# Performance work log

Hardware: AMD Instinct MI355X
Metric: run time of the kernel (lower is better)

## Reference

```python
import jax, jax.numpy as jnp
import numpy as np

D_MODEL = 512
N_HEADS = 8
HEAD_DIM = D_MODEL // N_HEADS
NEG_INF = -1e9


def setup_inputs() -> dict:
    key = jax.random.key(0)
    ks = jax.random.split(key, 12)
    B, N, M = 8, 2048, 2048
    inp = {
        'query': jax.random.normal(ks[0], (B, D_MODEL, N), jnp.float32),
        'key': jax.random.normal(ks[1], (B, D_MODEL, M), jnp.float32),
        'value': jax.random.normal(ks[2], (B, D_MODEL, M), jnp.float32),
        'query_mask': jnp.ones((B, N), jnp.float32),
        'key_value_mask': jnp.ones((B, M), jnp.float32),
        # Conv1d(d_model, d_model, kernel_size=1) == pointwise linear: W [out, in], b [out]
        'Wq': jax.random.normal(ks[3], (D_MODEL, D_MODEL), jnp.float32) / np.sqrt(D_MODEL),
        'bq': jax.random.normal(ks[4], (D_MODEL,), jnp.float32) * 0.01,
        'Wk': jax.random.normal(ks[5], (D_MODEL, D_MODEL), jnp.float32) / np.sqrt(D_MODEL),
        'bk': jax.random.normal(ks[6], (D_MODEL,), jnp.float32) * 0.01,
        'Wv': jax.random.normal(ks[7], (D_MODEL, D_MODEL), jnp.float32) / np.sqrt(D_MODEL),
        'bv': jax.random.normal(ks[8], (D_MODEL,), jnp.float32) * 0.01,
        'Wm': jax.random.normal(ks[9], (D_MODEL, D_MODEL), jnp.float32) / np.sqrt(D_MODEL),
        'bm': jax.random.normal(ks[10], (D_MODEL,), jnp.float32) * 0.01,
    }
    return inp


def _pointwise(W, b, x):
    # Conv1d k=1 over [B, C_in, N] -> [B, C_out, N]
    return jnp.einsum('oi,bin->bon', W, x) + b[None, :, None]


def reference(query, key, value, query_mask, key_value_mask,
              Wq, bq, Wk, bk, Wv, bv, Wm, bm):
    B = query.shape[0]
    N = query.shape[2]
    M = key.shape[2]
    # project and split heads: [B, head_dim, n_heads, seq]
    q = _pointwise(Wq, bq, query).reshape(B, HEAD_DIM, N_HEADS, N)
    k = _pointwise(Wk, bk, key).reshape(B, HEAD_DIM, N_HEADS, M)
    v = _pointwise(Wv, bv, value).reshape(B, HEAD_DIM, N_HEADS, M)
    # scores [B, H, N, M], scaled by sqrt(head_dim) (query.shape[1] post-split)
    scores = jnp.einsum('bdhn,bdhm->bhnm', q, k) / jnp.sqrt(jnp.float32(HEAD_DIM))
    # dual mask: outer product of key_value_mask [B,1,1,M] and query_mask [B,1,N,1]
    mask = key_value_mask[:, None, None, :] * query_mask[:, None, :, None]
    scores = jnp.where(mask > 0, scores, NEG_INF)
    prob = jax.nn.softmax(scores, axis=-1)  # [B, H, N, M]
    x = jnp.einsum('bhnm,bdhm->bdhn', prob, v)  # [B, head_dim, H, N]
    out = _pointwise(Wm, bm, x.reshape(B, D_MODEL, N))
    return out
```

## Files before the change

kernel.cpp:

```cpp
#include <hip/hip_runtime.h>


typedef _Float16 f16;
typedef _Float16 f16x4 __attribute__((ext_vector_type(4)));
typedef _Float16 f16x8 __attribute__((ext_vector_type(8)));
typedef float f32x4 __attribute__((ext_vector_type(4)));

#define D_MODEL 512
#define HD 64
#define SEQ 2048
#define QSCL 0.18033688011112042f
#define KVNEG -1.4426950409e9f
#define FMAXB -6.0f

__global__ __launch_bounds__(256) void k_transpose(
    const float* __restrict__ q, const float* __restrict__ k, const float* __restrict__ v,
    f16* __restrict__ XT)
{
  __shared__ __align__(16) f16 Ts[64][72];
  int t = threadIdx.x;
  int nt = blockIdx.x, ct = blockIdx.y, z = blockIdx.z;
  int src = z >> 3, b = z & 7;
  const float* S = (src == 0) ? q : (src == 1) ? k : v;
  {
    int cr = t >> 2, ns = t & 3;
    const float* p = S + ((size_t)b * D_MODEL + ct * 64 + cr) * SEQ + nt * 64 + ns * 16;
    f32x4 a0 = *(const f32x4*)(p);
    f32x4 a1 = *(const f32x4*)(p + 4);
    f32x4 a2 = *(const f32x4*)(p + 8);
    f32x4 a3 = *(const f32x4*)(p + 12);
    f16x8 h0, h1;
#pragma unroll
    for (int j = 0; j < 4; ++j) { h0[j] = (f16)a0[j]; h0[4 + j] = (f16)a1[j]; h1[j] = (f16)a2[j]; h1[4 + j] = (f16)a3[j]; }
    *(f16x8*)&Ts[cr][ns * 16] = h0;
    *(f16x8*)&Ts[cr][ns * 16 + 8] = h1;
  }
  __syncthreads();
  {
    int nr = t >> 2, cs = t & 3;
    f16x8 h0, h1;
#pragma unroll
    for (int j = 0; j < 8; ++j) h0[j] = Ts[cs * 16 + j][nr];
#pragma unroll
    for (int j = 0; j < 8; ++j) h1[j] = Ts[cs * 16 + 8 + j][nr];
    f16* dst = XT + (((size_t)z) * SEQ + nt * 64 + nr) * D_MODEL + ct * 64 + cs * 16;
    *(f16x8*)dst = h0;
    *(f16x8*)(dst + 8) = h1;
  }
}

__global__ __launch_bounds__(256) void k_wconv(
    const float* __restrict__ Wq, const float* __restrict__ Wk, const float* __restrict__ Wv,
    const float* __restrict__ Wm, f16* __restrict__ W3, f16* __restrict__ Wmh)
{
  int idx = blockIdx.x * 256 + threadIdx.x;
  if (idx < 262144) {
    W3[idx] = (f16)Wq[idx];
    W3[262144 + idx] = (f16)Wk[idx];
    W3[524288 + idx] = (f16)Wv[idx];
    int o = idx >> 9, c = idx & 511;
    int h = c & 7, d = c >> 3;
    Wmh[((size_t)h * 512 + o) * 64 + d] = (f16)Wm[idx];
  }
}

__global__ __launch_bounds__(256, 2) void k_proj(
    const f16* __restrict__ W3, const float* __restrict__ bq, const float* __restrict__ bk,
    const float* __restrict__ bv, const f16* __restrict__ XT,
    f16* __restrict__ Qt, f16* __restrict__ Kt, f16* __restrict__ Vh)
{
  __shared__ __align__(16) char smem[36864];
  f16 (*As)[72] = (f16(*)[72])smem;
  f16 (*Bs)[72] = (f16(*)[72])(smem + 18432);
  f16 (*Ls)[136] = (f16(*)[136])smem;

  int t = threadIdx.x;
  int proj = blockIdx.z, b = blockIdx.y;
  int ot = blockIdx.x & 3, ntile = blockIdx.x >> 2;
  int w = t >> 6, ln = t & 63, i16 = ln & 15, q4 = ln >> 4;
  int ow = w >> 1, nw = w & 1;

  const f16* Wp = W3 + (size_t)proj * 262144;
  const f16* Xp = XT + ((size_t)proj * 8 + b) * (size_t)SEQ * D_MODEL;

  f32x4 acc[4][4];
#pragma unroll
  for (int x = 0; x < 4; ++x)
#pragma unroll
    for (int y = 0; y < 4; ++y) acc[x][y] = (f32x4){0.f, 0.f, 0.f, 0.f};

  int srow = t >> 1, shalf = t & 1;
  for (int kc = 0; kc < 8; ++kc) {
    __syncthreads();
    const f16* Ap = Wp + ((size_t)(ot * 128 + srow)) * 512 + kc * 64 + shalf * 32;
#pragma unroll
    for (int s8 = 0; s8 < 4; ++s8)
      *(f32x4*)&As[srow][shalf * 32 + s8 * 8] = *(const f32x4*)(Ap + s8 * 8);
    const f16* Bp = Xp + ((size_t)(ntile * 128 + srow)) * 512 + kc * 64 + shalf * 32;
#pragma unroll
    for (int s8 = 0; s8 < 4; ++s8)
      *(f32x4*)&Bs[srow][shalf * 32 + s8 * 8] = *(const f32x4*)(Bp + s8 * 8);
    __syncthreads();
#pragma unroll
    for (int kk = 0; kk < 2; ++kk) {
      f16x8 af[4], bf[4];
#pragma unroll
      for (int x = 0; x < 4; ++x) af[x] = *(const f16x8*)&As[ow * 64 + x * 16 + i16][kk * 32 + q4 * 8];
#pragma unroll
      for (int y = 0; y < 4; ++y) bf[y] = *(const f16x8*)&Bs[nw * 64 + y * 16 + i16][kk * 32 + q4 * 8];
#pragma unroll
      for (int x = 0; x < 4; ++x)
#pragma unroll
        for (int y = 0; y < 4; ++y)
          acc[x][y] = __builtin_amdgcn_mfma_f32_16x16x32_f16(af[x], bf[y], acc[x][y], 0, 0, 0);
    }
  }

  const float* bias = (proj == 0) ? bq : (proj == 1) ? bk : bv;
  float scl = (proj == 0) ? QSCL : 1.0f;
  __syncthreads();
#pragma unroll
  for (int x = 0; x < 4; ++x) {
    f32x4 bb = *(const f32x4*)(bias + ot * 128 + ow * 64 + x * 16 + q4 * 4);
#pragma unroll
    for (int y = 0; y < 4; ++y)
#pragma unroll
      for (int r = 0; r < 4; ++r)
        Ls[ow * 64 + x * 16 + q4 * 4 + r][nw * 64 + y * 16 + i16] = (f16)((acc[x][y][r] + bb[r]) * scl);
  }
  __syncthreads();
  if (proj < 2) {
    f16* dst = (proj == 0) ? Qt : Kt;
    int n = t >> 1, seg = t & 1;
#pragma unroll
    for (int h = 0; h < 8; ++h) {
      f16x8 g;
#pragma unroll
      for (int j = 0; j < 8; ++j) g[j] = Ls[8 * (seg * 8 + j) + h][n];
      f16* dp = dst + (((size_t)((b * 8 + h) * 4 + ot)) * 2048 + ntile * 128 + n) * 16 + seg * 8;
      *(f16x8*)dp = g;
    }
  } else {
#pragma unroll
    for (int p = 0; p < 8; ++p) {
      int ol = (t >> 4) + 16 * p;
      int ch = t & 15;
      int og = ot * 128 + ol;
      int h = og & 7, d = og >> 3;
      f16* dp = Vh + (((size_t)(b * 8 + h)) * HD + d) * SEQ + ntile * 128 + ch * 8;
      *(f32x4*)dp = *(const f32x4*)&Ls[ol][ch * 8];
    }
  }
}

__global__ __launch_bounds__(256, 4) void k_attn(
    const f16* __restrict__ Qt, const f16* __restrict__ Kt, const f16* __restrict__ Vh,
    const float* __restrict__ qmask, const float* __restrict__ kvmask,
    f16* __restrict__ O)
{
  __shared__ __align__(16) char smem[18432];
  f16 (*Qs)[72] = (f16(*)[72])smem;
  f16 (*Ks)[72] = (f16(*)[72])smem;
  f16 (*Vs)[72] = (f16(*)[72])(smem + 9216);

  int t = threadIdx.x;
  int bh = blockIdx.x >> 4;
  int b = bh >> 3;
  int n0 = (blockIdx.x & 15) * 128;
  int w = t >> 6, ln = t & 63, i16 = ln & 15, q4 = ln >> 4;

  const f16* Qb = Qt + (size_t)bh * 131072;
  const f16* Kb = Kt + (size_t)bh * 131072;
  const f16* Vb = Vh + (size_t)bh * HD * SEQ;
  const float* kvp = kvmask + (size_t)b * SEQ;

  int tid0 = t, tid1 = 256 + t;
  int cx0 = tid0 >> 6, nk0 = tid0 & 63;
  int cx1 = tid1 >> 6, nk1 = tid1 & 63;
  int rk0 = (nk0 & 32) | ((nk0 & 4) << 2) | ((nk0 >> 1) & 12) | (nk0 & 3);
  int rk1 = (nk1 & 32) | ((nk1 & 4) << 2) | ((nk1 >> 1) & 12) | (nk1 & 3);
  int vw0 = tid0 >> 3, vc0 = tid0 & 7;
  int vw1 = tid1 >> 3, vc1 = tid1 & 7;
  const f16* ksp0 = Kb + ((size_t)((cx0 >> 1) * 2048 + nk0)) * 16 + (cx0 & 1) * 8;
  const f16* ksp1 = Kb + ((size_t)((cx1 >> 1) * 2048 + nk1)) * 16 + (cx1 & 1) * 8;
  const f16* vsp0 = Vb + (size_t)vw0 * SEQ + vc0 * 8;
  const f16* vsp1 = Vb + (size_t)vw1 * SEQ + vc1 * 8;

  f32x4 kA = *(const f32x4*)(ksp0);
  f32x4 kB = *(const f32x4*)(ksp1);
  f32x4 vA = *(const f32x4*)(vsp0);
  f32x4 vB = *(const f32x4*)(vsp1);

#pragma unroll
  for (int p = 0; p < 4; ++p) {
    int tid = p * 256 + t;
    int n = tid & 127, cx = tid >> 7;
    *(f32x4*)&Qs[n][cx * 8] =
        *(const f32x4*)(Qb + ((size_t)((cx >> 1) * 2048 + n0 + n)) * 16 + (cx & 1) * 8);
  }
  __syncthreads();
  f16x8 qf[2][2];
#pragma unroll
  for (int nt = 0; nt < 2; ++nt)
#pragma unroll
    for (int kc = 0; kc < 2; ++kc)
      qf[nt][kc] = *(const f16x8*)&Qs[w * 32 + nt * 16 + i16][kc * 32 + q4 * 8];
#pragma unroll
  for (int nt = 0; nt < 2; ++nt) {
    float qok = qmask[(size_t)b * SEQ + n0 + w * 32 + nt * 16 + i16];
    f16 qz = (qok > 0.f) ? (f16)1 : (f16)0;
    qf[nt][0] *= qz;
    qf[nt][1] *= qz;
  }

  f32x4 acc_o[4][2];
#pragma unroll
  for (int dt = 0; dt < 4; ++dt)
#pragma unroll
    for (int nt = 0; nt < 2; ++nt) acc_o[dt][nt] = (f32x4){0.f, 0.f, 0.f, 0.f};
  float rsum2[2] = {0.f, 0.f};

  for (int it = 0; it < 32; ++it) {
    int m0 = it * 64;
    __syncthreads();
    *(f32x4*)&Ks[rk0][cx0 * 8] = kA;
    *(f32x4*)&Ks[rk1][cx1 * 8] = kB;
    *(f32x4*)&Vs[vw0][vc0 * 8] = vA;
    *(f32x4*)&Vs[vw1][vc1 * 8] = vB;
    __syncthreads();
    if (it < 31) {
      int mo = (it + 1) * 64;
      kA = *(const f32x4*)(ksp0 + (size_t)mo * 16);
      kB = *(const f32x4*)(ksp1 + (size_t)mo * 16);
      vA = *(const f32x4*)(vsp0 + mo);
      vB = *(const f32x4*)(vsp1 + mo);
    }

    f32x4 bias[4];
#pragma unroll
    for (int mt = 0; mt < 4; ++mt) {
      f32x4 kv = *(const f32x4*)(kvp + m0 + ((mt >> 1) << 5) + ((mt & 1) << 2) + q4 * 8);
#pragma unroll
      for (int r = 0; r < 4; ++r) bias[mt][r] = (kv[r] > 0.f) ? FMAXB : KVNEG;
    }

    f32x4 s[2][4];
    __builtin_amdgcn_s_setprio(1);
#pragma unroll
    for (int mt = 0; mt < 4; ++mt) {
      f16x8 kf0 = *(const f16x8*)&Ks[mt * 16 + i16][q4 * 8];
      f16x8 kf1 = *(const f16x8*)&Ks[mt * 16 + i16][32 + q4 * 8];
      f32x4 a0 = __builtin_amdgcn_mfma_f32_16x16x32_f16(kf0, qf[0][0], bias[mt], 0, 0, 0);
      s[0][mt] = __builtin_amdgcn_mfma_f32_16x16x32_f16(kf1, qf[0][1], a0, 0, 0, 0);
      f32x4 a1 = __builtin_amdgcn_mfma_f32_16x16x32_f16(kf0, qf[1][0], bias[mt], 0, 0, 0);
      s[1][mt] = __builtin_amdgcn_mfma_f32_16x16x32_f16(kf1, qf[1][1], a1, 0, 0, 0);
    }
    __builtin_amdgcn_s_setprio(0);

    f16x8 pf[2][2];
#pragma unroll
    for (int nt = 0; nt < 2; ++nt) {
      float rs = 0.f;
#pragma unroll
      for (int mtp = 0; mtp < 2; ++mtp) {
        f16x8 pv;
#pragma unroll
        for (int r = 0; r < 4; ++r) {
          float p0 = __builtin_amdgcn_exp2f(s[nt][2 * mtp][r]);
          float p1 = __builtin_amdgcn_exp2f(s[nt][2 * mtp + 1][r]);
          rs += p0 + p1;
          pv[r] = (f16)p0;
          pv[4 + r] = (f16)p1;
        }
        pf[mtp][nt] = pv;
      }
      rsum2[nt] += rs;
    }

    __builtin_amdgcn_s_setprio(1);
#pragma unroll
    for (int dt = 0; dt < 4; ++dt) {
      f16x8 vf0 = *(const f16x8*)&Vs[dt * 16 + i16][q4 * 8];
      f16x8 vf1 = *(const f16x8*)&Vs[dt * 16 + i16][32 + q4 * 8];
#pragma unroll
      for (int nt = 0; nt < 2; ++nt) {
        f32x4 o = acc_o[dt][nt];
        o = __builtin_amdgcn_mfma_f32_16x16x32_f16(vf0, pf[0][nt], o, 0, 0, 0);
        o = __builtin_amdgcn_mfma_f32_16x16x32_f16(vf1, pf[1][nt], o, 0, 0, 0);
        acc_o[dt][nt] = o;
      }
    }
    __builtin_amdgcn_s_setprio(0);
  }

  __syncthreads();
  f16 (*Os)[72] = (f16(*)[72])(smem + w * 4608);
#pragma unroll
  for (int nt = 0; nt < 2; ++nt) {
    float l = rsum2[nt];
    l += __shfl_xor(l, 16, 64);
    l += __shfl_xor(l, 32, 64);
    float inv = 1.f / l;
#pragma unroll
    for (int dt = 0; dt < 4; ++dt) {
      f16x4 o4;
#pragma unroll
      for (int r = 0; r < 4; ++r) o4[r] = (f16)(acc_o[dt][nt][r] * inv);
      *(f16x4*)&Os[nt * 16 + i16][dt * 16 + q4 * 4] = o4;
    }
  }
  __syncthreads();
  f16* Ob = O + ((size_t)bh * SEQ + n0 + w * 32) * HD;
#pragma unroll
  for (int p = 0; p < 4; ++p) {
    int row = (ln >> 3) + 8 * p, ch = ln & 7;
    *(f32x4*)(Ob + (size_t)row * HD + ch * 8) = *(const f32x4*)&Os[row][ch * 8];
  }
}

__global__ __launch_bounds__(256, 2) void k_out(
    const f16* __restrict__ Wmh, const float* __restrict__ bm,
    const f16* __restrict__ O, float* __restrict__ out)
{
  __shared__ __align__(16) char smem[20480];
  f16 (*As)[40] = (f16(*)[40])smem;
  f16 (*Bs)[40] = (f16(*)[40])(smem + 10240);

  int t = threadIdx.x;
  int b = blockIdx.y;
  int ot = blockIdx.x & 3, ntile = blockIdx.x >> 2;
  int w = t >> 6, ln = t & 63, i16 = ln & 15, q4 = ln >> 4;
  int ow = w >> 1, nw = w & 1;

  f32x4 acc[4][4];
#pragma unroll
  for (int x = 0; x < 4; ++x)
#pragma unroll
    for (int y = 0; y < 4; ++y) acc[x][y] = (f32x4){0.f, 0.f, 0.f, 0.f};

  int srow = t >> 1, sseg = t & 1;
  for (int ck = 0; ck < 16; ++ck) {
    int h = ck >> 1, dc = ck & 1;
    __syncthreads();
    const f16* Ap = Wmh + ((size_t)h * 512 + ot * 128 + srow) * 64 + dc * 32 + sseg * 16;
    *(f32x4*)&As[srow][sseg * 16] = *(const f32x4*)(Ap);
    *(f32x4*)&As[srow][sseg * 16 + 8] = *(const f32x4*)(Ap + 8);
    const f16* Bp = O + (((size_t)(b * 8 + h)) * SEQ + ntile * 128 + srow) * 64 + dc * 32 + sseg * 16;
    *(f32x4*)&Bs[srow][sseg * 16] = *(const f32x4*)(Bp);
    *(f32x4*)&Bs[srow][sseg * 16 + 8] = *(const f32x4*)(Bp + 8);
    __syncthreads();
    f16x8 af[4], bf[4];
#pragma unroll
    for (int x = 0; x < 4; ++x) af[x] = *(const f16x8*)&As[ow * 64 + x * 16 + i16][q4 * 8];
#pragma unroll
    for (int y = 0; y < 4; ++y) bf[y] = *(const f16x8*)&Bs[nw * 64 + y * 16 + i16][q4 * 8];
#pragma unroll
    for (int x = 0; x < 4; ++x)
#pragma unroll
      for (int y = 0; y < 4; ++y)
        acc[x][y] = __builtin_amdgcn_mfma_f32_16x16x32_f16(af[x], bf[y], acc[x][y], 0, 0, 0);
  }

#pragma unroll
  for (int x = 0; x < 4; ++x) {
    f32x4 bb = *(const f32x4*)(bm + ot * 128 + ow * 64 + x * 16 + q4 * 4);
#pragma unroll
    for (int y = 0; y < 4; ++y)
#pragma unroll
      for (int r = 0; r < 4; ++r) {
        int o_g = ot * 128 + ow * 64 + x * 16 + q4 * 4 + r;
        int n_g = ntile * 128 + nw * 64 + y * 16 + i16;
        out[((size_t)b * 512 + o_g) * SEQ + n_g] = acc[x][y][r] + bb[r];
      }
  }
}

extern "C" void kernel_launch(void* const* d_in, const int* in_sizes, int n_in,
                              void* d_out, int out_size, void* d_ws, size_t ws_size,
                              hipStream_t stream)
{
  const float* query  = (const float*)d_in[0];
  const float* key    = (const float*)d_in[1];
  const float* value  = (const float*)d_in[2];
  const float* qmask  = (const float*)d_in[3];
  const float* kvmask = (const float*)d_in[4];
  const float* Wq = (const float*)d_in[5];
  const float* bq = (const float*)d_in[6];
  const float* Wk = (const float*)d_in[7];
  const float* bk = (const float*)d_in[8];
  const float* Wv = (const float*)d_in[9];
  const float* bv = (const float*)d_in[10];
  const float* Wm = (const float*)d_in[11];
  const float* bm = (const float*)d_in[12];
  float* out = (float*)d_out;

  char* ws = (char*)d_ws;
  f16* XT  = (f16*)(ws);
  f16* Qt  = (f16*)(ws + 50331648);
  f16* Kt  = (f16*)(ws + 67108864);
  f16* Vh  = (f16*)(ws + 83886080);
  f16* Oat = (f16*)(ws);
  f16* W3  = (f16*)(ws + 100663296);
  f16* Wmh = (f16*)(ws + 102236160);

  k_transpose<<<dim3(32, 8, 24), 256, 0, stream>>>(query, key, value, XT);
  k_wconv<<<1024, 256, 0, stream>>>(Wq, Wk, Wv, Wm, W3, Wmh);
  k_proj<<<dim3(64, 8, 3), 256, 0, stream>>>(W3, bq, bk, bv, XT, Qt, Kt, Vh);
  k_attn<<<1024, 256, 0, stream>>>(Qt, Kt, Vh, qmask, kvmask, Oat);
  k_out<<<dim3(64, 8), 256, 0, stream>>>(Wmh, bm, Oat, out);
}
```

Measured before the change: 329.2 us.

## Double-buffer K/V tiles in attention and precompute mask bias array

The attention loop now ping-pongs between two K/V shared-memory buffers, using one barrier per iteration instead of two, with the global prefetch running two tiles ahead. The key/value mask bias is precomputed once in the weight-conversion kernel into a scratch array held in the output buffer, so the inner loop loads bias values instead of comparing mask values. The QK MFMA and exp work is interleaved in two halves to overlap math with softmax. Shared memory doubles to 36 KB per block, which may reduce occupancy; reusing the output buffer as scratch relies on k_out overwriting it later.

```diff
diff --git a/kernel.cpp b/kernel.cpp
--- a/kernel.cpp
+++ b/kernel.cpp
@@ -51,7 +51,8 @@
 
 __global__ __launch_bounds__(256) void k_wconv(
     const float* __restrict__ Wq, const float* __restrict__ Wk, const float* __restrict__ Wv,
-    const float* __restrict__ Wm, f16* __restrict__ W3, f16* __restrict__ Wmh)
+    const float* __restrict__ Wm, const float* __restrict__ kvmask,
+    f16* __restrict__ W3, f16* __restrict__ Wmh, float* __restrict__ biasArr)
 {
   int idx = blockIdx.x * 256 + threadIdx.x;
   if (idx < 262144) {
@@ -62,6 +63,9 @@
     int h = c & 7, d = c >> 3;
     Wmh[((size_t)h * 512 + o) * 64 + d] = (f16)Wm[idx];
   }
+  if (idx < 16384) {
+    biasArr[idx] = (kvmask[idx] > 0.f) ? FMAXB : KVNEG;
+  }
 }
 
 __global__ __launch_bounds__(256, 2) void k_proj(
@@ -155,13 +159,15 @@
 
 __global__ __launch_bounds__(256, 4) void k_attn(
     const f16* __restrict__ Qt, const f16* __restrict__ Kt, const f16* __restrict__ Vh,
-    const float* __restrict__ qmask, const float* __restrict__ kvmask,
+    const float* __restrict__ qmask, const float* __restrict__ biasArr,
     f16* __restrict__ O)
 {
-  __shared__ __align__(16) char smem[18432];
+  __shared__ __align__(16) char smem[36864];
   f16 (*Qs)[72] = (f16(*)[72])smem;
-  f16 (*Ks)[72] = (f16(*)[72])smem;
-  f16 (*Vs)[72] = (f16(*)[72])(smem + 9216);
+  f16 (*Ks0)[72] = (f16(*)[72])(smem);
+  f16 (*Vs0)[72] = (f16(*)[72])(smem + 9216);
+  f16 (*Ks1)[72] = (f16(*)[72])(smem + 18432);
+  f16 (*Vs1)[72] = (f16(*)[72])(smem + 27648);
 
   int t = threadIdx.x;
   int bh = blockIdx.x >> 4;
@@ -172,7 +178,7 @@
   const f16* Qb = Qt + (size_t)bh * 131072;
   const f16* Kb = Kt + (size_t)bh * 131072;
   const f16* Vb = Vh + (size_t)bh * HD * SEQ;
-  const float* kvp = kvmask + (size_t)b * SEQ;
+  const float* bap = biasArr + (size_t)b * SEQ;
 
   int tid0 = t, tid1 = 256 + t;
   int cx0 = tid0 >> 6, nk0 = tid0 & 63;
@@ -212,6 +218,17 @@
     qf[nt][0] *= qz;
     qf[nt][1] *= qz;
   }
+  __syncthreads();
+
+  *(f32x4*)&Ks0[rk0][cx0 * 8] = kA;
+  *(f32x4*)&Ks0[rk1][cx1 * 8] = kB;
+  *(f32x4*)&Vs0[vw0][vc0 * 8] = vA;
+  *(f32x4*)&Vs0[vw1][vc1 * 8] = vB;
+  kA = *(const f32x4*)(ksp0 + (size_t)64 * 16);
+  kB = *(const f32x4*)(ksp1 + (size_t)64 * 16);
+  vA = *(const f32x4*)(vsp0 + 64);
+  vB = *(const f32x4*)(vsp1 + 64);
+  __syncthreads();
 
   f32x4 acc_o[4][2];
 #pragma unroll
@@ -220,68 +237,65 @@
     for (int nt = 0; nt < 2; ++nt) acc_o[dt][nt] = (f32x4){0.f, 0.f, 0.f, 0.f};
   float rsum2[2] = {0.f, 0.f};
 
-  for (int it = 0; it < 32; ++it) {
-    int m0 = it * 64;
-    __syncthreads();
-    *(f32x4*)&Ks[rk0][cx0 * 8] = kA;
-    *(f32x4*)&Ks[rk1][cx1 * 8] = kB;
-    *(f32x4*)&Vs[vw0][vc0 * 8] = vA;
-    *(f32x4*)&Vs[vw1][vc1 * 8] = vB;
-    __syncthreads();
+  auto body = [&](int it, f16 (*Kc)[72], f16 (*Vc)[72], f16 (*Kn)[72], f16 (*Vn)[72]) {
     if (it < 31) {
-      int mo = (it + 1) * 64;
+      *(f32x4*)&Kn[rk0][cx0 * 8] = kA;
+      *(f32x4*)&Kn[rk1][cx1 * 8] = kB;
+      *(f32x4*)&Vn[vw0][vc0 * 8] = vA;
+      *(f32x4*)&Vn[vw1][vc1 * 8] = vB;
+    }
+    if (it < 30) {
+      int mo = (it + 2) * 64;
       kA = *(const f32x4*)(ksp0 + (size_t)mo * 16);
       kB = *(const f32x4*)(ksp1 + (size_t)mo * 16);
       vA = *(const f32x4*)(vsp0 + mo);
       vB = *(const f32x4*)(vsp1 + mo);
     }
-
-    f32x4 bias[4];
-#pragma unroll
-    for (int mt = 0; mt < 4; ++mt) {
-      f32x4 kv = *(const f32x4*)(kvp + m0 + ((mt >> 1) << 5) + ((mt & 1) << 2) + q4 * 8);
-#pragma unroll
-      for (int r = 0; r < 4; ++r) bias[mt][r] = (kv[r] > 0.f) ? FMAXB : KVNEG;
-    }
-
-    f32x4 s[2][4];
+    int m0 = it * 64;
+
+    f16x8 pf[2][2];
+    float rs0 = 0.f, rs1 = 0.f;
+#pragma unroll
+    for (int p = 0; p < 2; ++p) {
+      f32x4 bias0 = *(const f32x4*)(bap + m0 + p * 32 + q4 * 8);
+      f32x4 bias1 = *(const f32x4*)(bap + m0 + p * 32 + 4 + q4 * 8);
+      f16x8 kf00 = *(const f16x8*)&Kc[(2 * p) * 16 + i16][q4 * 8];
+      f16x8 kf01 = *(const f16x8*)&Kc[(2 * p) * 16 + i16][32 + q4 * 8];
+      f16x8 kf10 = *(const f16x8*)&Kc[(2 * p + 1) * 16 + i16][q4 * 8];
+      f16x8 kf11 = *(const f16x8*)&Kc[(2 * p + 1) * 16 + i16][32 + q4 * 8];
+      __builtin_amdgcn_s_setprio(1);
+      f32x4 s00 = __builtin_amdgcn_mfma_f32_16x16x32_f16(kf00, qf[0][0], bias0, 0, 0, 0);
+      s00 = __builtin_amdgcn_mfma_f32_16x16x32_f16(kf01, qf[0][1], s00, 0, 0, 0);
+      f32x4 s01 = __builtin_amdgcn_mfma_f32_16x16x32_f16(kf10, qf[0][0], bias1, 0, 0, 0);
+      s01 = __builtin_amdgcn_mfma_f32_16x16x32_f16(kf11, qf[0][1], s01, 0, 0, 0);
+      f32x4 s10 = __builtin_amdgcn_mfma_f32_16x16x32_f16(kf00, qf[1][0], bias0, 0, 0, 0);
+      s10 = __builtin_amdgcn_mfma_f32_16x16x32_f16(kf01, qf[1][1], s10, 0, 0, 0);
+      f32x4 s11 = __builtin_amdgcn_mfma_f32_16x16x32_f16(kf10, qf[1][0], bias1, 0, 0, 0);
+      s11 = __builtin_amdgcn_mfma_f32_16x16x32_f16(kf11, qf[1][1], s11, 0, 0, 0);
+      __builtin_amdgcn_s_setprio(0);
+      f16x8 pv0, pv1;
+#pragma unroll
+      for (int r = 0; r < 4; ++r) {
+        float e00 = __builtin_amdgcn_exp2f(s00[r]);
+        float e01 = __builtin_amdgcn_exp2f(s01[r]);
+        float e10 = __builtin_amdgcn_exp2f(s10[r]);
+        float e11 = __builtin_amdgcn_exp2f(s11[r]);
+        rs0 += e00 + e01;
+        rs1 += e10 + e11;
+        pv0[r] = (f16)e00; pv0[4 + r] = (f16)e01;
+        pv1[r] = (f16)e10; pv1[4 + r] = (f16)e11;
+      }
+      pf[p][0] = pv0;
+      pf[p][1] = pv1;
+    }
+    rsum2[0] += rs0;
+    rsum2[1] += rs1;
+
     __builtin_amdgcn_s_setprio(1);
 #pragma unroll
-    for (int mt = 0; mt < 4; ++mt) {
-      f16x8 kf0 = *(const f16x8*)&Ks[mt * 16 + i16][q4 * 8];
-      f16x8 kf1 = *(const f16x8*)&Ks[mt * 16 + i16][32 + q4 * 8];
-      f32x4 a0 = __builtin_amdgcn_mfma_f32_16x16x32_f16(kf0, qf[0][0], bias[mt], 0, 0, 0);
-      s[0][mt] = __builtin_amdgcn_mfma_f32_16x16x32_f16(kf1, qf[0][1], a0, 0, 0, 0);
-      f32x4 a1 = __builtin_amdgcn_mfma_f32_16x16x32_f16(kf0, qf[1][0], bias[mt], 0, 0, 0);
-      s[1][mt] = __builtin_amdgcn_mfma_f32_16x16x32_f16(kf1, qf[1][1], a1, 0, 0, 0);
-    }
-    __builtin_amdgcn_s_setprio(0);
-
-    f16x8 pf[2][2];
-#pragma unroll
-    for (int nt = 0; nt < 2; ++nt) {
-      float rs = 0.f;
-#pragma unroll
-      for (int mtp = 0; mtp < 2; ++mtp) {
-        f16x8 pv;
-#pragma unroll
-        for (int r = 0; r < 4; ++r) {
-          float p0 = __builtin_amdgcn_exp2f(s[nt][2 * mtp][r]);
-          float p1 = __builtin_amdgcn_exp2f(s[nt][2 * mtp + 1][r]);
-          rs += p0 + p1;
-          pv[r] = (f16)p0;
-          pv[4 + r] = (f16)p1;
-        }
-        pf[mtp][nt] = pv;
-      }
-      rsum2[nt] += rs;
-    }
-
-    __builtin_amdgcn_s_setprio(1);
-#pragma unroll
     for (int dt = 0; dt < 4; ++dt) {
-      f16x8 vf0 = *(const f16x8*)&Vs[dt * 16 + i16][q4 * 8];
-      f16x8 vf1 = *(const f16x8*)&Vs[dt * 16 + i16][32 + q4 * 8];
+      f16x8 vf0 = *(const f16x8*)&Vc[dt * 16 + i16][q4 * 8];
+      f16x8 vf1 = *(const f16x8*)&Vc[dt * 16 + i16][32 + q4 * 8];
 #pragma unroll
       for (int nt = 0; nt < 2; ++nt) {
         f32x4 o = acc_o[dt][nt];
@@ -291,9 +305,14 @@
       }
     }
     __builtin_amdgcn_s_setprio(0);
-  }
-
-  __syncthreads();
+    __syncthreads();
+  };
+
+  for (int ot = 0; ot < 16; ++ot) {
+    body(2 * ot, Ks0, Vs0, Ks1, Vs1);
+    body(2 * ot + 1, Ks1, Vs1, Ks0, Vs0);
+  }
+
   f16 (*Os)[72] = (f16(*)[72])(smem + w * 4608);
 #pragma unroll
   for (int nt = 0; nt < 2; ++nt) {
@@ -402,10 +421,11 @@
   f16* Oat = (f16*)(ws);
   f16* W3  = (f16*)(ws + 100663296);
   f16* Wmh = (f16*)(ws + 102236160);
+  float* biasArr = out;
 
   k_transpose<<<dim3(32, 8, 24), 256, 0, stream>>>(query, key, value, XT);
-  k_wconv<<<1024, 256, 0, stream>>>(Wq, Wk, Wv, Wm, W3, Wmh);
+  k_wconv<<<1024, 256, 0, stream>>>(Wq, Wk, Wv, Wm, kvmask, W3, Wmh, biasArr);
   k_proj<<<dim3(64, 8, 3), 256, 0, stream>>>(W3, bq, bk, bv, XT, Qt, Kt, Vh);
-  k_attn<<<1024, 256, 0, stream>>>(Qt, Kt, Vh, qmask, kvmask, Oat);
+  k_attn<<<1024, 256, 0, stream>>>(Qt, Kt, Vh, qmask, biasArr, Oat);
   k_out<<<dim3(64, 8), 256, 0, stream>>>(Wmh, bm, Oat, out);
 }
```

Measured after the change: 391.4 us. +18.9%, slower.
